# Kernel optimization log

Hardware: AMD Instinct MI355X
Metric: run time of the kernel (lower is better)

Reference implementation:

```python
import jax, jax.numpy as jnp
import numpy as np

N_NODES = 100000
EPS = 1e-12


def gcn_conv(x, src, dst, ew, W, b, n):
    """PyG GCNConv with edge weights: add self-loops (w=1), symmetric norm,
    scatter-add messages from src to dst, then bias."""
    loop = jnp.arange(n)
    src2 = jnp.concatenate([src, loop])
    dst2 = jnp.concatenate([dst, loop])
    ew2 = jnp.concatenate([ew, jnp.ones((n,), dtype=ew.dtype)])
    deg = jax.ops.segment_sum(ew2, dst2, num_segments=n)
    dinv = jnp.where(deg > 0, jax.lax.rsqrt(jnp.where(deg > 0, deg, 1.0)), 0.0)
    norm = dinv[src2] * ew2 * dinv[dst2]  # [E+N]
    xw = x @ W.T                           # [N, H]
    msg = xw[src2] * norm[:, None]         # [E+N, H]  (memory-bound gather)
    out = jax.ops.segment_sum(msg, dst2, num_segments=n)
    return out + b


def setup_inputs() -> dict:
    key = jax.random.key(0)
    ks = jax.random.split(key, 12)
    N, E, D_IN, H, FE = N_NODES, 1600000, 256, 128, 8
    x = jax.random.normal(ks[0], (N, D_IN), dtype=jnp.float32)
    edge_index = jax.random.randint(ks[1], (2, E), 0, N, dtype=jnp.int64)
    edge_attr = jax.random.uniform(ks[2], (E, FE), dtype=jnp.float32)
    s_in = 1.0 / np.sqrt(D_IN)
    s_h = 1.0 / np.sqrt(H)
    W_in = jax.random.uniform(ks[3], (H, D_IN), minval=-s_in, maxval=s_in)
    b_in = jax.random.uniform(ks[4], (H,), minval=-s_in, maxval=s_in)
    W1 = jax.random.uniform(ks[5], (H, H), minval=-s_h, maxval=s_h)
    b1 = jax.random.uniform(ks[6], (H,), minval=-s_h, maxval=s_h)
    W2 = jax.random.uniform(ks[7], (H, H), minval=-s_h, maxval=s_h)
    b2 = jax.random.uniform(ks[8], (H,), minval=-s_h, maxval=s_h)
    W_out = jax.random.uniform(ks[9], (H, H), minval=-s_h, maxval=s_h)
    b_out = jax.random.uniform(ks[10], (H,), minval=-s_h, maxval=s_h)
    return {"x": x, "edge_index": edge_index, "edge_attr": edge_attr,
            "W_in": W_in, "b_in": b_in, "W1": W1, "b1": b1,
            "W2": W2, "b2": b2, "W_out": W_out, "b_out": b_out}


def reference(x, edge_index, edge_attr, W_in, b_in, W1, b1, W2, b2, W_out, b_out):
    n = x.shape[0]
    src, dst = edge_index[0], edge_index[1]
    # edge weights: sum over edge features, then L2-normalize over edges
    ew = edge_attr.sum(axis=1)
    ew = ew / jnp.maximum(jnp.linalg.norm(ew), EPS)
    h = jax.nn.relu(x @ W_in.T + b_in)      # dropout = identity (eval)
    h = jax.nn.relu(gcn_conv(h, src, dst, ew, W1, b1, n))
    h = gcn_conv(h, src, dst, ew, W2, b2, n)
    return h @ W_out.T + b_out
```

## Files before the change

### kernel.cpp

```cpp
#include <hip/hip_runtime.h>
#include <hip/hip_bf16.h>
#include <math.h>


#define CAP 64
#define BN 256
#define BCAP 5120
#define CHUNK 4096
#define NBMAX 400
#define SRC_MASK 0x1FFFFu
#define Q_SCALE 16777216.0f
#define Q_INV   5.9604644775390625e-8f
#define GSTRIDE 1024

typedef __attribute__((ext_vector_type(8))) short bf16x8;
typedef __attribute__((ext_vector_type(2))) float f32x2;
typedef __attribute__((ext_vector_type(4))) float f32x4;
typedef __attribute__((ext_vector_type(4))) unsigned int u32x4;

#if __has_builtin(__builtin_amdgcn_cvt_pk_f32_fp8)
#define DEC_SCALE 5.9604644775390625e-8f
__device__ __forceinline__ f32x2 dec2(unsigned short t) {
  return __builtin_amdgcn_cvt_pk_f32_fp8((int)(unsigned)t, false);
}
#else
#define DEC_SCALE 7.922816251426434e28f
__device__ __forceinline__ f32x2 dec2(unsigned short t) {
  f32x2 r;
  r.x = __builtin_bit_cast(float, (((unsigned)t & 0x80u) << 24) | (((unsigned)t & 0x7Fu) << 20));
  r.y = __builtin_bit_cast(float, (((unsigned)t & 0x8000u) << 16) | (((unsigned)t & 0x7F00u) << 12));
  return r;
}
#endif

__device__ __forceinline__ unsigned rne_bf16(float f) {
  const unsigned u = __builtin_bit_cast(unsigned, f);
  return (u + 0x7FFFu + ((u >> 16) & 1u)) >> 16;
}
__device__ __forceinline__ unsigned packsplit(float f) {
  const unsigned hb = rne_bf16(f);
  const float hf = __builtin_bit_cast(float, hb << 16);
  const unsigned lb = rne_bf16(f - hf);
  return (hb << 16) | (lb & 0xFFFFu);
}
__device__ __forceinline__ float unpk(unsigned p) {
  return __builtin_bit_cast(float, p & 0xFFFF0000u) +
         __builtin_bit_cast(float, p << 16);
}
__device__ __forceinline__ void split8(const f32x4 a, const f32x4 b,
                                       bf16x8& hi, bf16x8& lo) {
#pragma unroll
  for (int i = 0; i < 8; ++i) {
    const float f = (i < 4) ? a[i] : b[i - 4];
    const unsigned hb = rne_bf16(f);
    hi[i] = (short)hb;
    const float hf = __builtin_bit_cast(float, hb << 16);
    lo[i] = (short)rne_bf16(f - hf);
  }
}
__device__ __forceinline__ unsigned char enc_e4m3(float v) {
  const float a = v * 0x1p-120f;
  unsigned bits = __builtin_bit_cast(unsigned, a);
  const unsigned sgn = (bits >> 24) & 0x80u;
  bits &= 0x7FFFFFFFu;
  unsigned u7 = (bits + 0x7FFFFu + ((bits >> 20) & 1u)) >> 20;
  if (u7 > 0x7Eu) u7 = 0x7Eu;
  return (unsigned char)(sgn | u7);
}

__global__ void ew_wsplit_kernel(const float* __restrict__ ea, float* __restrict__ ew,
                                 float* __restrict__ partial, int E,
                                 const float* __restrict__ W_in, const float* __restrict__ W1,
                                 const float* __restrict__ W2, const float* __restrict__ W_out,
                                 short* __restrict__ whi, short* __restrict__ wlo) {
  __shared__ float red[256];
  const int tid = threadIdx.x;
  if (blockIdx.x < 1024) {
    float ss = 0.f;
    const int stride = 1024 * 256;
    for (int e = blockIdx.x * 256 + tid; e < E; e += stride) {
      const float4 a = *(const float4*)(ea + (size_t)e * 8);
      const float4 b = *(const float4*)(ea + (size_t)e * 8 + 4);
      const float s = ((a.x + a.y) + (a.z + a.w)) + ((b.x + b.y) + (b.z + b.w));
      ew[e] = s;
      ss = fmaf(s, s, ss);
    }
    red[tid] = ss;
    __syncthreads();
    for (int k = 128; k > 0; k >>= 1) {
      if (tid < k) red[tid] += red[tid + k];
      __syncthreads();
    }
    if (tid == 0) partial[blockIdx.x] = red[0];
  } else {
    const int i = (blockIdx.x - 1024) * 256 + tid;
    if (i < 81920) {
      float f;
      if (i < 32768) f = W_in[i];
      else if (i < 49152) f = W1[i - 32768];
      else if (i < 65536) f = W2[i - 49152];
      else f = W_out[i - 65536];
      const unsigned hb = rne_bf16(f);
      whi[i] = (short)hb;
      wlo[i] = (short)rne_bf16(f - __builtin_bit_cast(float, hb << 16));
    }
  }
}

__global__ void norm_cursor_kernel(const float* __restrict__ partial,
                                   float* __restrict__ invnorm,
                                   unsigned* __restrict__ cursors, int NB) {
  __shared__ float red[256];
  const int tid = threadIdx.x;
  if (blockIdx.x == 0) {
    float s = partial[tid] + partial[tid + 256] + partial[tid + 512] + partial[tid + 768];
    red[tid] = s;
    __syncthreads();
    for (int k = 128; k > 0; k >>= 1) {
      if (tid < k) red[tid] += red[tid + k];
      __syncthreads();
    }
    if (tid == 0) invnorm[0] = 1.0f / fmaxf(sqrtf(red[0]), 1e-12f);
  } else {
    const int i = (blockIdx.x - 1) * 256 + tid;
    if (i < NB) cursors[i * 16] = (unsigned)i * BCAP;
  }
}

__global__ __launch_bounds__(512, 4) void bin_gemmin_kernel(
    const int* __restrict__ src, const int* __restrict__ dst,
    const float* __restrict__ ew, const float* __restrict__ invnorm,
    unsigned* __restrict__ cursors, unsigned long long* __restrict__ buckets,
    int E, int NB, int nbin,
    const float* __restrict__ X, const short* __restrict__ Whi,
    const short* __restrict__ Wlo, const float* __restrict__ bias,
    unsigned* __restrict__ Ypk, int ntiles) {
  __shared__ __align__(16) char smem[53952];
  __shared__ unsigned wsb[8];
  const int tid = threadIdx.x;
  if ((int)blockIdx.x < nbin) {
    unsigned long long* recs = (unsigned long long*)smem;
    unsigned* perm = (unsigned*)(smem + 32768);
    unsigned* hist = (unsigned*)(smem + 49152);
    unsigned* base = (unsigned*)(smem + 50752);
    unsigned* lofs = (unsigned*)(smem + 52352);
    const int e0 = blockIdx.x * CHUNK;
    const int n = min(CHUNK, E - e0);
    for (int i = tid; i < NBMAX; i += 512) hist[i] = 0;
    __syncthreads();
    const float inv = invnorm[0];
    for (int i = tid; i < n; i += 512) {
      const int s = src[e0 + i];
      const int d = dst[e0 + i];
      const float w = ew[e0 + i] * inv;
      const unsigned q = (unsigned)fminf(fmaf(w, Q_SCALE, 0.5f), 32767.0f);
      recs[i] = ((unsigned long long)(((unsigned)d << 15) | q) << 32) | (unsigned)s;
      atomicAdd(&hist[d >> 8], 1u);
    }
    __syncthreads();
    {
      const unsigned x = (tid < NB) ? hist[tid] : 0u;
      unsigned xi = x;
#pragma unroll
      for (int d = 1; d < 64; d <<= 1) {
        const unsigned y = __shfl_up(xi, d, 64);
        if ((tid & 63) >= d) xi += y;
      }
      if ((tid & 63) == 63) wsb[tid >> 6] = xi;
      __syncthreads();
      if (tid == 0) {
        unsigned s = 0;
        for (int w2 = 0; w2 < 8; ++w2) { const unsigned t = wsb[w2]; wsb[w2] = s; s += t; }
      }
      __syncthreads();
      if (tid < NB) {
        lofs[tid] = wsb[tid >> 6] + xi - x;
        base[tid] = x ? atomicAdd(&cursors[tid * 16], x) : 0u;
        hist[tid] = 0;
      }
    }
    __syncthreads();
    for (int i = tid; i < n; i += 512) {
      const unsigned b = (unsigned)(recs[i] >> 55);
      const unsigned rank = atomicAdd(&hist[b], 1u);
      perm[lofs[b] + rank] = (b << 12) | (unsigned)i;
    }
    __syncthreads();
    for (int p = tid; p < n; p += 512) {
      const unsigned u = perm[p];
      const unsigned b = u >> 12;
      const unsigned g = base[b] + ((unsigned)p - lofs[b]);
      if (g < (b + 1) * BCAP) buckets[g] = recs[u & 4095u];
    }
  } else {
    constexpr int K = 256, KT = 8, RT = 2, CPR = 32;
    short* hi_p = (short*)smem;
    short* lo_p = (short*)(smem + 16384);
    const int lane = tid & 63, wave = tid >> 6;
    const int lrow = lane & 15, loct = lane >> 4;

    bf16x8 bhi[KT], blo[KT];
    const int col = wave * 16 + lrow;
#pragma unroll
    for (int kt = 0; kt < KT; ++kt) {
      const int off = col * K + kt * 32 + loct * 8;
      bhi[kt] = *(const bf16x8*)&Whi[off];
      blo[kt] = *(const bf16x8*)&Wlo[off];
    }
    const float bv = bias[col];

    const int r0c = tid >> 5, r1c = (tid + 512) >> 5;
    const int cc = tid & 31;
    f32x4 sa[2][2];
    const int vb = (int)blockIdx.x - nbin;

    int t = vb;
    {
      const int tl = (t < ntiles) ? t : 0;
      const float* xp0 = X + ((size_t)tl * 32 + r0c) * K + cc * 8;
      const float* xp1 = X + ((size_t)tl * 32 + r1c) * K + cc * 8;
      sa[0][0] = *(const f32x4*)xp0; sa[0][1] = *(const f32x4*)(xp0 + 4);
      sa[1][0] = *(const f32x4*)xp1; sa[1][1] = *(const f32x4*)(xp1 + 4);
    }
    while (t < ntiles) {
      {
        const int slot0 = r0c * CPR + (cc ^ (r0c & 7));
        const int slot1 = r1c * CPR + (cc ^ (r1c & 7));
        bf16x8 h, l;
        split8(sa[0][0], sa[0][1], h, l);
        *(bf16x8*)&hi_p[slot0 * 8] = h;
        *(bf16x8*)&lo_p[slot0 * 8] = l;
        split8(sa[1][0], sa[1][1], h, l);
        *(bf16x8*)&hi_p[slot1 * 8] = h;
        *(bf16x8*)&lo_p[slot1 * 8] = l;
      }
      __syncthreads();
      const int tn = t + GSTRIDE;
      {
        const int tl = (tn < ntiles) ? tn : 0;
        const float* xp0 = X + ((size_t)tl * 32 + r0c) * K + cc * 8;
        const float* xp1 = X + ((size_t)tl * 32 + r1c) * K + cc * 8;
        sa[0][0] = *(const f32x4*)xp0; sa[0][1] = *(const f32x4*)(xp0 + 4);
        sa[1][0] = *(const f32x4*)xp1; sa[1][1] = *(const f32x4*)(xp1 + 4);
      }
      f32x4 acc[RT];
#pragma unroll
      for (int rt = 0; rt < RT; ++rt) acc[rt] = f32x4{0.f, 0.f, 0.f, 0.f};
#pragma unroll
      for (int kt = 0; kt < KT; ++kt) {
        bf16x8 ahi[RT], alo[RT];
#pragma unroll
        for (int rt = 0; rt < RT; ++rt) {
          const int lr = rt * 16 + lrow;
          const int off = (lr * CPR + ((kt * 4 + loct) ^ (lr & 7))) * 8;
          ahi[rt] = *(const bf16x8*)&hi_p[off];
          alo[rt] = *(const bf16x8*)&lo_p[off];
        }
#pragma unroll
        for (int rt = 0; rt < RT; ++rt) {
          acc[rt] = __builtin_amdgcn_mfma_f32_16x16x32_bf16(ahi[rt], bhi[kt], acc[rt], 0, 0, 0);
          acc[rt] = __builtin_amdgcn_mfma_f32_16x16x32_bf16(ahi[rt], blo[kt], acc[rt], 0, 0, 0);
          acc[rt] = __builtin_amdgcn_mfma_f32_16x16x32_bf16(alo[rt], bhi[kt], acc[rt], 0, 0, 0);
        }
      }
      const int rbase = t * 32;
#pragma unroll
      for (int rt = 0; rt < RT; ++rt)
#pragma unroll
        for (int r = 0; r < 4; ++r) {
          const float v = fmaxf(acc[rt][r] + bv, 0.f);
          Ypk[(size_t)(rbase + rt * 16 + loct * 4 + r) * 128 + col] = packsplit(v);
        }
      t = tn;
      __syncthreads();
    }
  }
}

__global__ __launch_bounds__(256) void build_kernel(
    const unsigned long long* __restrict__ buckets,
    const unsigned* __restrict__ cursors,
    unsigned* __restrict__ cv, float* __restrict__ dinv,
    int* __restrict__ fillg, int N) {
  __shared__ unsigned cvl[BN * CAP];
  __shared__ unsigned fl[BN];
  const int tid = threadIdx.x;
  const int b = blockIdx.x;
  const int n0 = b << 8;
  for (int i = tid; i < BN * CAP; i += 256) cvl[i] = 0;
  for (int i = tid; i < BN; i += 256) fl[i] = 0;
  __syncthreads();
  const unsigned start = (unsigned)b * BCAP;
  const int cnt = min((int)(cursors[b * 16] - start), BCAP);
  for (int i = tid; i < cnt; i += 256) {
    const unsigned long long r = buckets[start + i];
    const unsigned hi = (unsigned)(r >> 32);
    const unsigned dlo = (hi >> 15) & (BN - 1);
    const unsigned q = hi & 0x7FFFu;
    const unsigned p = atomicAdd(&fl[dlo], 1u);
    if (p < CAP) cvl[(dlo << 6) + p] = (q << 17) | (unsigned)(r & 0xFFFFFFFFu);
  }
  __syncthreads();
  if (n0 + tid < N) {
    const int c = min((int)fl[tid], CAP);
    unsigned qs = 0;
    for (int i = 0; i < c; ++i) qs += cvl[(tid << 6) + i] >> 17;
    dinv[n0 + tid] = rsqrtf(fmaf((float)qs, Q_INV, 1.0f));
    fillg[n0 + tid] = c;
  }
  const u32x4* s = (const u32x4*)cvl;
  u32x4* g = (u32x4*)(cv + ((size_t)b << 14));
  for (int i = tid; i < BN * CAP / 4; i += 256)
    __builtin_nontemporal_store(s[i], &g[i]);
}

template <bool OUT_FP8, bool OUT_F32, bool HAS_BIAS, bool RELU>
__device__ __forceinline__ void gemm_pk_body(
    char* smem, int vb, int stride,
    const unsigned* __restrict__ Xpk, const short* __restrict__ Whi,
    const short* __restrict__ Wlo, const float* __restrict__ bias,
    unsigned* __restrict__ Ypk, unsigned char* __restrict__ Yf8,
    float* __restrict__ Yf32, int ntiles) {
  constexpr int K = 128, KT = 4, CT = 2, RT = 2, CPR = 16;
  short* hi_p = (short*)smem;
  short* lo_p = (short*)(smem + 8192);
  const int tid = threadIdx.x;
  const int lane = tid & 63, wave = tid >> 6;
  const int lrow = lane & 15, loct = lane >> 4;

  bf16x8 bhi[CT][KT], blo[CT][KT];
#pragma unroll
  for (int ct = 0; ct < CT; ++ct) {
    const int col = (wave * CT + ct) * 16 + lrow;
#pragma unroll
    for (int kt = 0; kt < KT; ++kt) {
      const int off = col * K + kt * 32 + loct * 8;
      bhi[ct][kt] = *(const bf16x8*)&Whi[off];
      blo[ct][kt] = *(const bf16x8*)&Wlo[off];
    }
  }
  float bv[CT];
  if constexpr (HAS_BIAS) {
#pragma unroll
    for (int ct = 0; ct < CT; ++ct) bv[ct] = bias[(wave * CT + ct) * 16 + lrow];
  }

  const int r0c = tid >> 4, r1c = (tid + 256) >> 4;
  const int cc = tid & 15;
  u32x4 sa[2][2];

  int t = vb;
  {
    const int tl = (t < ntiles) ? t : 0;
    const unsigned* xp0 = Xpk + ((size_t)tl * 32 + r0c) * K + cc * 8;
    const unsigned* xp1 = Xpk + ((size_t)tl * 32 + r1c) * K + cc * 8;
    sa[0][0] = *(const u32x4*)xp0; sa[0][1] = *(const u32x4*)(xp0 + 4);
    sa[1][0] = *(const u32x4*)xp1; sa[1][1] = *(const u32x4*)(xp1 + 4);
  }
  while (t < ntiles) {
#pragma unroll
    for (int p = 0; p < 2; ++p) {
      const int r = p ? r1c : r0c;
      const int slot = r * CPR + (cc ^ (r & 7));
      const u32x4 a = sa[p][0], b = sa[p][1];
      u32x4 wh, wl;
      wh[0] = (a[1] & 0xFFFF0000u) | (a[0] >> 16);
      wh[1] = (a[3] & 0xFFFF0000u) | (a[2] >> 16);
      wh[2] = (b[1] & 0xFFFF0000u) | (b[0] >> 16);
      wh[3] = (b[3] & 0xFFFF0000u) | (b[2] >> 16);
      wl[0] = (a[1] << 16) | (a[0] & 0xFFFFu);
      wl[1] = (a[3] << 16) | (a[2] & 0xFFFFu);
      wl[2] = (b[1] << 16) | (b[0] & 0xFFFFu);
      wl[3] = (b[3] << 16) | (b[2] & 0xFFFFu);
      *(u32x4*)&hi_p[slot * 8] = wh;
      *(u32x4*)&lo_p[slot * 8] = wl;
    }
    __syncthreads();
    const int tn = t + stride;
    {
      const int tl = (tn < ntiles) ? tn : 0;
      const unsigned* xp0 = Xpk + ((size_t)tl * 32 + r0c) * K + cc * 8;
      const unsigned* xp1 = Xpk + ((size_t)tl * 32 + r1c) * K + cc * 8;
      sa[0][0] = *(const u32x4*)xp0; sa[0][1] = *(const u32x4*)(xp0 + 4);
      sa[1][0] = *(const u32x4*)xp1; sa[1][1] = *(const u32x4*)(xp1 + 4);
    }
    f32x4 acc[RT][CT];
#pragma unroll
    for (int rt = 0; rt < RT; ++rt)
#pragma unroll
      for (int ct = 0; ct < CT; ++ct) acc[rt][ct] = f32x4{0.f, 0.f, 0.f, 0.f};
#pragma unroll
    for (int kt = 0; kt < KT; ++kt) {
      bf16x8 ahi[RT], alo[RT];
#pragma unroll
      for (int rt = 0; rt < RT; ++rt) {
        const int lr = rt * 16 + lrow;
        const int off = (lr * CPR + ((kt * 4 + loct) ^ (lr & 7))) * 8;
        ahi[rt] = *(const bf16x8*)&hi_p[off];
        alo[rt] = *(const bf16x8*)&lo_p[off];
      }
#pragma unroll
      for (int rt = 0; rt < RT; ++rt)
#pragma unroll
        for (int ct = 0; ct < CT; ++ct) {
          acc[rt][ct] = __builtin_amdgcn_mfma_f32_16x16x32_bf16(ahi[rt], bhi[ct][kt], acc[rt][ct], 0, 0, 0);
          acc[rt][ct] = __builtin_amdgcn_mfma_f32_16x16x32_bf16(ahi[rt], blo[ct][kt], acc[rt][ct], 0, 0, 0);
          acc[rt][ct] = __builtin_amdgcn_mfma_f32_16x16x32_bf16(alo[rt], bhi[ct][kt], acc[rt][ct], 0, 0, 0);
        }
    }
    const int rbase = t * 32;
#pragma unroll
    for (int rt = 0; rt < RT; ++rt)
#pragma unroll
      for (int ct = 0; ct < CT; ++ct) {
        const int col = (wave * CT + ct) * 16 + lrow;
#pragma unroll
        for (int r = 0; r < 4; ++r) {
          float v = acc[rt][ct][r];
          if constexpr (HAS_BIAS) v += bv[ct];
          if constexpr (RELU) v = fmaxf(v, 0.f);
          const size_t idx = (size_t)(rbase + rt * 16 + loct * 4 + r) * 128 + col;
          if constexpr (OUT_F32) {
            Yf32[idx] = v;
          } else {
            Ypk[idx] = packsplit(v);
            if constexpr (OUT_FP8) Yf8[idx] = enc_e4m3(v);
          }
        }
      }
    t = tn;
    __syncthreads();
  }
}

__global__ __launch_bounds__(256, 4) void valfin_gemmpk_kernel(
    unsigned* __restrict__ cv, const int* __restrict__ fillg,
    const float* __restrict__ dinv, int N,
    const unsigned* __restrict__ Xpk, const short* __restrict__ Whi,
    const short* __restrict__ Wlo, unsigned* __restrict__ Ypk,
    unsigned char* __restrict__ Yf8, int ntiles) {
  __shared__ __align__(16) char smem[16384];
  if (blockIdx.x < 512) {
    const int total = N * (CAP / 4);
    for (int i = blockIdx.x * 256 + threadIdx.x; i < total; i += 512 * 256) {
      const int n = i >> 4;
      const int slot0 = (i & 15) * 4;
      const int c = fillg[n];
      if (slot0 >= c) continue;
      const float dn = dinv[n];
      u32x4 q = *(u32x4*)&cv[((size_t)n << 6) + slot0];
#pragma unroll
      for (int j = 0; j < 4; ++j) {
        if (slot0 + j < c) {
          const unsigned s = q[j] & SRC_MASK;
          const float wv = dinv[s] * dn * ((float)(q[j] >> 17) * Q_INV);
          const unsigned w15 = (unsigned)fminf(fmaf(wv, Q_SCALE, 0.5f), 32767.0f);
          q[j] = (w15 << 17) | s;
        }
      }
      *(u32x4*)&cv[((size_t)n << 6) + slot0] = q;
    }
  } else {
    gemm_pk_body<true, false, false, false>(smem, (int)blockIdx.x - 512, GSTRIDE,
                                            Xpk, Whi, Wlo, nullptr, Ypk, Yf8,
                                            nullptr, ntiles);
  }
}

template <bool OUT_FP8, bool OUT_F32, bool HAS_BIAS, bool RELU>
__global__ __launch_bounds__(256, 4) void gemm_pk_pipe(
    const unsigned* __restrict__ Xpk, const short* __restrict__ Whi,
    const short* __restrict__ Wlo, const float* __restrict__ bias,
    unsigned* __restrict__ Ypk, unsigned char* __restrict__ Yf8,
    float* __restrict__ Yf32, int ntiles) {
  __shared__ __align__(16) char smem[16384];
  gemm_pk_body<OUT_FP8, OUT_F32, HAS_BIAS, RELU>(smem, (int)blockIdx.x, GSTRIDE,
                                                 Xpk, Whi, Wlo, bias, Ypk, Yf8,
                                                 Yf32, ntiles);
}

template <bool RELU>
__global__ __launch_bounds__(256) void gather_kernel(const unsigned* __restrict__ xw,
                                                     const unsigned char* __restrict__ xf8,
                                                     const int* __restrict__ fill,
                                                     const unsigned* __restrict__ cv,
                                                     const float* __restrict__ dinv,
                                                     const float* __restrict__ bias,
                                                     unsigned* __restrict__ out, int N) {
  const int lane = threadIdx.x & 63;
  const int n = (blockIdx.x * blockDim.x + threadIdx.x) >> 6;
  if (n >= N) return;
  const int f = lane * 2;
  const float dn = dinv[n];
  const float dn2 = dn * dn;
  const uint2 xs = *(const uint2*)&xw[(size_t)n * 128 + f];
  float ax = dn2 * unpk(xs.x);
  float ay = dn2 * unpk(xs.y);
  const unsigned* row = cv + ((size_t)n << 6);
  const int c = min(fill[n], CAP);
  for (int e = 0; e < c; e += 16) {
    u32x4 cg[4];
    cg[0] = *(const u32x4*)&row[e];
    cg[1] = *(const u32x4*)&row[e + 4];
    cg[2] = *(const u32x4*)&row[e + 8];
    cg[3] = *(const u32x4*)&row[e + 12];
    unsigned cr[16];
#pragma unroll
    for (int g = 0; g < 4; ++g) {
      cr[g * 4 + 0] = cg[g][0]; cr[g * 4 + 1] = cg[g][1];
      cr[g * 4 + 2] = cg[g][2]; cr[g * 4 + 3] = cg[g][3];
    }
    unsigned short t[16];
#pragma unroll
    for (int j = 0; j < 16; ++j)
      t[j] = *(const unsigned short*)&xf8[(size_t)(cr[j] & SRC_MASK) * 128 + f];
#pragma unroll
    for (int j = 0; j < 16; ++j) {
      const float vs = (float)(cr[j] >> 17) * DEC_SCALE;
      const f32x2 xy = dec2(t[j]);
      ax = fmaf(vs, xy.x, ax);
      ay = fmaf(vs, xy.y, ay);
    }
  }
  const float2 bb = *(const float2*)&bias[f];
  float o0 = ax + bb.x, o1 = ay + bb.y;
  if (RELU) { o0 = fmaxf(o0, 0.f); o1 = fmaxf(o1, 0.f); }
  uint2 res;
  res.x = packsplit(o0);
  res.y = packsplit(o1);
  *(uint2*)&out[(size_t)n * 128 + f] = res;
}

extern "C" void kernel_launch(void* const* d_in, const int* in_sizes, int n_in,
                              void* d_out, int out_size, void* d_ws, size_t ws_size,
                              hipStream_t stream) {
  const float* x     = (const float*)d_in[0];
  const int*   eidx  = (const int*)d_in[1];
  const float* ea    = (const float*)d_in[2];
  const float* W_in  = (const float*)d_in[3];
  const float* b_in  = (const float*)d_in[4];
  const float* W1    = (const float*)d_in[5];
  const float* b1    = (const float*)d_in[6];
  const float* W2    = (const float*)d_in[7];
  const float* b2    = (const float*)d_in[8];
  const float* W_out = (const float*)d_in[9];
  const float* b_out = (const float*)d_in[10];

  const int E = in_sizes[2] / 8;
  const int N = in_sizes[0] / 256;
  const int* srcp = eidx;
  const int* dstp = eidx + E;
  const int NB = (N + BN - 1) / BN;
  const int nbin = (E + CHUNK - 1) / CHUNK;

  char* w = (char*)d_ws;
  size_t o = 0;
  auto take = [&](size_t bytes) -> void* {
    void* p = w + o;
    o += (bytes + 255) & ~(size_t)255;
    return p;
  };
  float* ew            = (float*)take((size_t)E * 4);
  float* partial       = (float*)take(1024 * 4);
  float* invnorm       = (float*)take(256);
  float* dinv          = (float*)take((size_t)N * 4);
  int*   fillg         = (int*)take((size_t)N * 4);
  short* whi           = (short*)take(81920 * 2);
  short* wlo           = (short*)take(81920 * 2);
  unsigned* cursors    = (unsigned*)take((size_t)NB * 16 * 4);
  unsigned long long* buckets = (unsigned long long*)take((size_t)NB * BCAP * 8);
  unsigned* cv         = (unsigned*)take((size_t)NB * BN * CAP * 4);
  unsigned* buf0       = (unsigned*)take((size_t)N * 128 * 4);
  unsigned* buf1       = (unsigned*)take((size_t)N * 128 * 4);
  unsigned char* buff8 = (unsigned char*)take((size_t)N * 128);
  float* outp          = (float*)d_out;

  const int ntiles = N / 32;

  ew_wsplit_kernel<<<1344, 256, 0, stream>>>(ea, ew, partial, E,
                                             W_in, W1, W2, W_out, whi, wlo);
  norm_cursor_kernel<<<1 + (NB + 255) / 256, 256, 0, stream>>>(partial, invnorm, cursors, NB);
  bin_gemmin_kernel<<<nbin + GSTRIDE, 512, 0, stream>>>(
      srcp, dstp, ew, invnorm, cursors, buckets, E, NB, nbin,
      x, whi, wlo, b_in, buf0, ntiles);
  build_kernel<<<NB, 256, 0, stream>>>(buckets, cursors, cv, dinv, fillg, N);
  valfin_gemmpk_kernel<<<512 + GSTRIDE, 256, 0, stream>>>(
      cv, fillg, dinv, N, buf0, whi + 32768, wlo + 32768, buf1, buff8, ntiles);
  gather_kernel<true><<<(N * 64 + 255) / 256, 256, 0, stream>>>(buf1, buff8, fillg, cv, dinv, b1, buf0, N);
  gemm_pk_pipe<true, false, false, false><<<GSTRIDE, 256, 0, stream>>>(
      buf0, whi + 49152, wlo + 49152, nullptr, buf1, buff8, nullptr, ntiles);
  gather_kernel<false><<<(N * 64 + 255) / 256, 256, 0, stream>>>(buf1, buff8, fillg, cv, dinv, b2, buf0, N);
  gemm_pk_pipe<false, true, true, false><<<GSTRIDE, 256, 0, stream>>>(
      buf0, whi + 65536, wlo + 65536, b_out, nullptr, nullptr, outp, ntiles);
}
```

Before: 277.2 us.

## Fold W_out into second GCN layer weights and drop final GEMM

```diff
diff --git a/kernel.cpp b/kernel.cpp
--- a/kernel.cpp
+++ b/kernel.cpp
@@ -68,10 +68,31 @@
   return (unsigned char)(sgn | u7);
 }
 
+__global__ void wfuse_kernel(const float* __restrict__ W2, const float* __restrict__ W_out,
+                             const float* __restrict__ b2, const float* __restrict__ b_out,
+                             float* __restrict__ Wf, float* __restrict__ bf) {
+  const int i = blockIdx.x * 256 + threadIdx.x;
+  if (i < 16384) {
+    const int j = i >> 7, p = i & 127;
+    const float* wo = W_out + j * 128;
+    float s = 0.f;
+#pragma unroll 8
+    for (int k = 0; k < 128; ++k) s = fmaf(wo[k], W2[k * 128 + p], s);
+    Wf[i] = s;
+  } else if (i < 16384 + 128) {
+    const int j = i - 16384;
+    const float* wo = W_out + j * 128;
+    float s = b_out[j];
+#pragma unroll 8
+    for (int k = 0; k < 128; ++k) s = fmaf(wo[k], b2[k], s);
+    bf[j] = s;
+  }
+}
+
 __global__ void ew_wsplit_kernel(const float* __restrict__ ea, float* __restrict__ ew,
                                  float* __restrict__ partial, int E,
                                  const float* __restrict__ W_in, const float* __restrict__ W1,
-                                 const float* __restrict__ W2, const float* __restrict__ W_out,
+                                 const float* __restrict__ Wf,
                                  short* __restrict__ whi, short* __restrict__ wlo) {
   __shared__ float red[256];
   const int tid = threadIdx.x;
@@ -94,12 +115,11 @@
     if (tid == 0) partial[blockIdx.x] = red[0];
   } else {
     const int i = (blockIdx.x - 1024) * 256 + tid;
-    if (i < 81920) {
+    if (i < 65536) {
       float f;
       if (i < 32768) f = W_in[i];
       else if (i < 49152) f = W1[i - 32768];
-      else if (i < 65536) f = W2[i - 49152];
-      else f = W_out[i - 65536];
+      else f = Wf[i - 49152];
       const unsigned hb = rne_bf16(f);
       whi[i] = (short)hb;
       wlo[i] = (short)rne_bf16(f - __builtin_bit_cast(float, hb << 16));
@@ -479,14 +499,15 @@
                                                  Yf32, ntiles);
 }
 
-template <bool RELU>
+template <bool RELU, bool OUT_F32>
 __global__ __launch_bounds__(256) void gather_kernel(const unsigned* __restrict__ xw,
                                                      const unsigned char* __restrict__ xf8,
                                                      const int* __restrict__ fill,
                                                      const unsigned* __restrict__ cv,
                                                      const float* __restrict__ dinv,
                                                      const float* __restrict__ bias,
-                                                     unsigned* __restrict__ out, int N) {
+                                                     unsigned* __restrict__ out,
+                                                     float* __restrict__ outf, int N) {
   const int lane = threadIdx.x & 63;
   const int n = (blockIdx.x * blockDim.x + threadIdx.x) >> 6;
   if (n >= N) return;
@@ -525,10 +546,16 @@
   const float2 bb = *(const float2*)&bias[f];
   float o0 = ax + bb.x, o1 = ay + bb.y;
   if (RELU) { o0 = fmaxf(o0, 0.f); o1 = fmaxf(o1, 0.f); }
-  uint2 res;
-  res.x = packsplit(o0);
-  res.y = packsplit(o1);
-  *(uint2*)&out[(size_t)n * 128 + f] = res;
+  if constexpr (OUT_F32) {
+    float2 res;
+    res.x = o0; res.y = o1;
+    *(float2*)&outf[(size_t)n * 128 + f] = res;
+  } else {
+    uint2 res;
+    res.x = packsplit(o0);
+    res.y = packsplit(o1);
+    *(uint2*)&out[(size_t)n * 128 + f] = res;
+  }
 }
 
 extern "C" void kernel_launch(void* const* d_in, const int* in_sizes, int n_in,
@@ -565,8 +592,10 @@
   float* invnorm       = (float*)take(256);
   float* dinv          = (float*)take((size_t)N * 4);
   int*   fillg         = (int*)take((size_t)N * 4);
-  short* whi           = (short*)take(81920 * 2);
-  short* wlo           = (short*)take(81920 * 2);
+  float* Wfused        = (float*)take(16384 * 4);
+  float* bfused        = (float*)take(128 * 4);
+  short* whi           = (short*)take(65536 * 2);
+  short* wlo           = (short*)take(65536 * 2);
   unsigned* cursors    = (unsigned*)take((size_t)NB * 16 * 4);
   unsigned long long* buckets = (unsigned long long*)take((size_t)NB * BCAP * 8);
   unsigned* cv         = (unsigned*)take((size_t)NB * BN * CAP * 4);
@@ -577,8 +606,9 @@
 
   const int ntiles = N / 32;
 
-  ew_wsplit_kernel<<<1344, 256, 0, stream>>>(ea, ew, partial, E,
-                                             W_in, W1, W2, W_out, whi, wlo);
+  wfuse_kernel<<<65, 256, 0, stream>>>(W2, W_out, b2, b_out, Wfused, bfused);
+  ew_wsplit_kernel<<<1280, 256, 0, stream>>>(ea, ew, partial, E,
+                                             W_in, W1, Wfused, whi, wlo);
   norm_cursor_kernel<<<1 + (NB + 255) / 256, 256, 0, stream>>>(partial, invnorm, cursors, NB);
   bin_gemmin_kernel<<<nbin + GSTRIDE, 512, 0, stream>>>(
       srcp, dstp, ew, invnorm, cursors, buckets, E, NB, nbin,
@@ -586,10 +616,10 @@
   build_kernel<<<NB, 256, 0, stream>>>(buckets, cursors, cv, dinv, fillg, N);
   valfin_gemmpk_kernel<<<512 + GSTRIDE, 256, 0, stream>>>(
       cv, fillg, dinv, N, buf0, whi + 32768, wlo + 32768, buf1, buff8, ntiles);
-  gather_kernel<true><<<(N * 64 + 255) / 256, 256, 0, stream>>>(buf1, buff8, fillg, cv, dinv, b1, buf0, N);
+  gather_kernel<true, false><<<(N * 64 + 255) / 256, 256, 0, stream>>>(
+      buf1, buff8, fillg, cv, dinv, b1, buf0, nullptr, N);
   gemm_pk_pipe<true, false, false, false><<<GSTRIDE, 256, 0, stream>>>(
       buf0, whi + 49152, wlo + 49152, nullptr, buf1, buff8, nullptr, ntiles);
-  gather_kernel<false><<<(N * 64 + 255) / 256, 256, 0, stream>>>(buf1, buff8, fillg, cv, dinv, b2, buf0, N);
-  gemm_pk_pipe<false, true, true, false><<<GSTRIDE, 256, 0, stream>>>(
-      buf0, whi + 65536, wlo + 65536, b_out, nullptr, nullptr, outp, ntiles);
-}
+  gather_kernel<false, true><<<(N * 64 + 255) / 256, 256, 0, stream>>>(
+      buf1, buff8, fillg, cv, dinv, bfused, nullptr, outp, N);
+}
```

Result: faster. 264.7 us, median of 2 (-4.5%).
